# Performance work log

Measured on AMD Instinct MI355X. Metric: run time of the kernel, lower is better.

## Reference

```python
import jax, jax.numpy as jnp
import numpy as np

N = 50000      # nodes
E = 800000     # edges
F_IN = 256     # feat_dim
H = 256        # hidden dim (both layers)
L = 128        # latent dim
BN_EPS = 1e-5


def setup_inputs() -> dict:
    key = jax.random.key(0)
    ks = jax.random.split(key, 16)
    x = jax.random.normal(ks[0], (N, F_IN), dtype=jnp.float32)
    edge_index = jax.random.randint(ks[1], (2, E), 0, N, dtype=jnp.int32)
    s = 0.05
    return {
        "x": x,
        "edge_index": edge_index,
        "W0": s * jax.random.normal(ks[2], (F_IN, H), jnp.float32),
        "b0": jnp.zeros((H,), jnp.float32),
        "gamma0": jnp.ones((H,), jnp.float32),
        "beta0": jnp.zeros((H,), jnp.float32),
        "W1": s * jax.random.normal(ks[3], (H, H), jnp.float32),
        "b1": jnp.zeros((H,), jnp.float32),
        "gamma1": jnp.ones((H,), jnp.float32),
        "beta1": jnp.zeros((H,), jnp.float32),
        "W_mu": s * jax.random.normal(ks[4], (H, L), jnp.float32),
        "b_mu": jnp.zeros((L,), jnp.float32),
        "W_lv": s * jax.random.normal(ks[5], (H, L), jnp.float32),
        "b_lv": jnp.zeros((L,), jnp.float32),
    }


def _gcn_conv(h, src, dst, coef, W, b):
    # h' = W h, then symmetric-normalized scatter-add aggregation (PyG GCNConv)
    h = h @ W                                   # [N, H]
    msg = h[src] * coef                         # gather + scale, [E+N, H]
    out = jax.ops.segment_sum(msg, dst, num_segments=N)
    return out + b


def _bn(h, gamma, beta):
    # BatchNorm1d over node dimension (training-mode batch statistics)
    m = h.mean(axis=0)
    v = h.var(axis=0)
    return (h - m) * jax.lax.rsqrt(v + BN_EPS) * gamma + beta


def reference(x, edge_index, W0, b0, gamma0, beta0, W1, b1, gamma1, beta1,
              W_mu, b_mu, W_lv, b_lv):
    loops = jnp.arange(N, dtype=edge_index.dtype)
    src = jnp.concatenate([edge_index[0], loops])   # with self-loops
    dst = jnp.concatenate([edge_index[1], loops])
    deg = jax.ops.segment_sum(jnp.ones((E + N,), x.dtype), dst, num_segments=N)
    dinv = jnp.where(deg > 0, jax.lax.rsqrt(jnp.maximum(deg, 1.0)), 0.0)
    coef = (dinv[src] * dinv[dst])[:, None]          # [E+N, 1]

    h = jax.nn.relu(_bn(_gcn_conv(x, src, dst, coef, W0, b0), gamma0, beta0))
    h = jax.nn.relu(_bn(_gcn_conv(h, src, dst, coef, W1, b1), gamma1, beta1))
    # dropout is identity at inference
    mu = h @ W_mu + b_mu
    logvar = h @ W_lv + b_lv
    return mu, logvar
```

## Files before the change

kernel.cpp:

```cpp
#include <hip/hip_runtime.h>
#include <hip/hip_bf16.h>

#define NN 50000
#define NP 50001
#define NE 800000
#define FD 256
#define LD 128
#define BN_EPS 1e-5f
#define NEPAD (NE + 7 * NN + 16)
#define CNT_BLKS 3125
#define ORD_BLKS 196
#define SCAN_BLKS 49

typedef __bf16 bf16_t;
typedef bf16_t bf16x8 __attribute__((ext_vector_type(8)));
typedef float f32x4 __attribute__((ext_vector_type(4)));
typedef float f32x2 __attribute__((ext_vector_type(2)));
typedef int i32x2 __attribute__((ext_vector_type(2)));
typedef int i32x4 __attribute__((ext_vector_type(4)));
typedef unsigned int u32x4 __attribute__((ext_vector_type(4)));
typedef unsigned short u16x8 __attribute__((ext_vector_type(8)));

__global__ __launch_bounds__(256) void k_countw(
    const int* __restrict__ dst, int* __restrict__ cnt,
    const float* __restrict__ W0, const float* __restrict__ W1,
    const float* __restrict__ Wmu, const float* __restrict__ bmu,
    const float* __restrict__ Wlv, const float* __restrict__ blv,
    bf16_t* __restrict__ W0s, bf16_t* __restrict__ W1s,
    bf16_t* __restrict__ Whs, float* __restrict__ biash,
    bf16_t* __restrict__ g16, bf16_t* __restrict__ agg16) {
  int b = blockIdx.x, t = threadIdx.x;
  if (b < CNT_BLKS) {
    int i = b * 256 + t;
    if (i < NE) atomicAdd(&cnt[dst[i]], 1);
  } else {
    int k = b - CNT_BLKS, n = t;
    int chunk = (n >> 4) * 8 + (k >> 5);
    int slot = ((k >> 3) & 3) * 16 + (n & 15);
    int idx = chunk * 512 + slot * 8 + (k & 7);
    W0s[idx] = (bf16_t)W0[k * 256 + n];
    W1s[idx] = (bf16_t)W1[k * 256 + n];
    float wh = (n < 128) ? Wmu[k * 128 + n] : Wlv[k * 128 + (n - 128)];
    Whs[idx] = (bf16_t)wh;
    if (k == 0) biash[n] = (n < 128) ? bmu[n] : blv[n - 128];
    if (k == 1) {
      int ss = n >> 6, j = n & 63;
      g16[((size_t)ss * NP + NN) * 64 + j] = (bf16_t)0.f;
      agg16[((size_t)ss * NP + NN) * 64 + j] = (bf16_t)0.f;
    }
  }
}

__global__ __launch_bounds__(256) void k_scanA(const int* __restrict__ cnt,
                                               int* __restrict__ row_ptr,
                                               int* __restrict__ partials,
                                               float* __restrict__ dinv) {
  __shared__ int ws[4];
  int b = blockIdx.x, t = threadIdx.x;
  int base = b * 1024 + t * 4;
  int vals[4];
#pragma unroll
  for (int j = 0; j < 4; ++j) {
    int deg = (base + j < NN) ? cnt[base + j] : 0;
    vals[j] = (base + j < NN) ? ((deg + 7) & ~7) : 0;
    if (base + j < NN) dinv[base + j] = rsqrtf(1.0f + (float)deg);
  }
  int tsum = vals[0] + vals[1] + vals[2] + vals[3];
  int lane = t & 63, wid = t >> 6;
  int x = tsum;
#pragma unroll
  for (int off = 1; off < 64; off <<= 1) {
    int y = __shfl_up(x, off, 64);
    if (lane >= off) x += y;
  }
  if (lane == 63) ws[wid] = x;
  __syncthreads();
  int woff = 0;
  for (int w = 0; w < wid; ++w) woff += ws[w];
  int run = woff + x - tsum;
#pragma unroll
  for (int j = 0; j < 4; ++j) {
    if (base + j < NN) row_ptr[base + j] = run;
    run += vals[j];
  }
  if (t == 255) partials[b] = woff + x;
}

__global__ void k_scanB(int* __restrict__ partials, int* __restrict__ row_ptr) {
  int lane = threadIdx.x;
  int v = (lane < SCAN_BLKS) ? partials[lane] : 0;
  int x = v;
#pragma unroll
  for (int off = 1; off < 64; off <<= 1) {
    int y = __shfl_up(x, off, 64);
    if (lane >= off) x += y;
  }
  if (lane < SCAN_BLKS) partials[lane] = x - v;
  if (lane == SCAN_BLKS - 1) row_ptr[NN] = x;
}

__global__ __launch_bounds__(256) void k_scanC(int* __restrict__ row_ptr,
                                               const int* __restrict__ partials,
                                               const int* __restrict__ cnt,
                                               unsigned short* __restrict__ col,
                                               int* __restrict__ hist) {
  __shared__ int lh[64];
  int b = blockIdx.x, t = threadIdx.x;
  if (t < 64) lh[t] = 0;
  __syncthreads();
  int off = partials[b];
  int base = b * 1024 + t * 4;
#pragma unroll
  for (int j = 0; j < 4; ++j)
    if (base + j < NN) {
      int deg = cnt[base + j];
      int rp = row_ptr[base + j] + off;
      row_ptr[base + j] = rp;
      int pd = (deg + 7) & ~7;
      for (int p = deg; p < pd; ++p) col[rp + p] = (unsigned short)NN;
      int it = pd >> 3;
      if (it > 63) it = 63;
      atomicAdd(&lh[63 - it], 1);
    }
  __syncthreads();
  if (t < 64 && lh[t]) atomicAdd(&hist[t], lh[t]);
}

__global__ __launch_bounds__(256) void k_fillorder(
    const int* __restrict__ src, const int* __restrict__ dst,
    const int* __restrict__ row_ptr, int* __restrict__ cursor,
    unsigned short* __restrict__ col, const int* __restrict__ cnt,
    const float* __restrict__ dinv, const int* __restrict__ hist,
    int* __restrict__ rank, int* __restrict__ order, i32x2* __restrict__ desc,
    float* __restrict__ dinvp) {
  int b = blockIdx.x, t = threadIdx.x;
  if (b < CNT_BLKS) {
    int i = b * 256 + t;
    if (i < NE) {
      int d = dst[i];
      int p = atomicAdd(&cursor[d], 1);
      col[row_ptr[d] + p] = (unsigned short)src[i];
    }
  } else {
    __shared__ int lcnt[64];
    __shared__ int gbase[64];
    __shared__ int sc[64];
    if (t < 64) {
      lcnt[t] = 0;
      int v = hist[t];
      int x = v;
#pragma unroll
      for (int off = 1; off < 64; off <<= 1) {
        int y = __shfl_up(x, off, 64);
        if (t >= off) x += y;
      }
      sc[t] = x - v;
    }
    __syncthreads();
    int i = (b - CNT_BLKS) * 256 + t;
    int bin = 0, rloc = 0, pd = 0;
    bool valid = (i < NN);
    if (valid) {
      pd = (cnt[i] + 7) & ~7;
      int it = pd >> 3;
      if (it > 63) it = 63;
      bin = 63 - it;
      rloc = atomicAdd(&lcnt[bin], 1);
    }
    __syncthreads();
    if (t < 64 && lcnt[t]) gbase[t] = sc[t] + atomicAdd(&rank[t], lcnt[t]);
    __syncthreads();
    if (valid) {
      int p = gbase[bin] + rloc;
      order[p] = i;
      int rp = row_ptr[i];
      desc[p] = (i32x2){rp, rp + pd};
      dinvp[p] = dinv[i];
    }
  }
}

__global__ __launch_bounds__(512) void k_mgemm(
    const void* __restrict__ Ap, int a_f32, const bf16_t* __restrict__ Wswz,
    bf16_t* __restrict__ Cb, float* __restrict__ Cf, int M,
    const float* __restrict__ stats, const float* __restrict__ gamma,
    const float* __restrict__ beta, const float* __restrict__ row_scale,
    const float* __restrict__ col_bias, int split) {
  __shared__ bf16_t Ws[64 * 512];
  __shared__ float bnsc_l[256], bnsh_l[256];
  const int tid = threadIdx.x;
  const int half = blockIdx.y;
  {
    const bf16_t* srcW = Wswz + (size_t)half * 64 * 512;
    bf16x8 wraw[8];
#pragma unroll
    for (int i = 0; i < 8; ++i)
      wraw[i] = *(const bf16x8*)&srcW[(i * 512 + tid) * 8];
#pragma unroll
    for (int i = 0; i < 8; ++i) *(bf16x8*)&Ws[(i * 512 + tid) * 8] = wraw[i];
  }
  if (stats && tid < 256) {
    float mean = stats[tid] * (1.0f / NN);
    float var = stats[256 + tid] * (1.0f / NN) - mean * mean;
    float rs = rsqrtf(var + BN_EPS);
    float sc = gamma[tid] * rs;
    bnsc_l[tid] = sc;
    bnsh_l[tid] = beta[tid] - mean * sc;
  }
  __syncthreads();

  const int wave = tid >> 6, lane = tid & 63;
  const int m = lane & 15, q = lane >> 4;
  const int row0 = blockIdx.x * 128 + wave * 16;
  const int rg = row0 + m;
  const int rc = rg < M ? rg : M - 1;

  bf16x8 af[8];
  if (a_f32) {
    const float* p = (const float*)Ap + (size_t)rc * 256 + q * 8;
    float4 f0[8], f1[8];
#pragma unroll
    for (int kb = 0; kb < 8; ++kb) {
      f0[kb] = *(const float4*)(p + kb * 32);
      f1[kb] = *(const float4*)(p + kb * 32 + 4);
    }
#pragma unroll
    for (int kb = 0; kb < 8; ++kb) {
      bf16x8 fr;
      fr[0] = (bf16_t)f0[kb].x; fr[1] = (bf16_t)f0[kb].y;
      fr[2] = (bf16_t)f0[kb].z; fr[3] = (bf16_t)f0[kb].w;
      fr[4] = (bf16_t)f1[kb].x; fr[5] = (bf16_t)f1[kb].y;
      fr[6] = (bf16_t)f1[kb].z; fr[7] = (bf16_t)f1[kb].w;
      af[kb] = fr;
    }
  } else {
    const bf16_t* pA = (const bf16_t*)Ap;
    bf16x8 raw[8];
#pragma unroll
    for (int kb = 0; kb < 8; ++kb)
      raw[kb] = *(const bf16x8*)&pA[((size_t)(kb >> 1) * NP + rc) * 64 +
                                    (kb & 1) * 32 + q * 8];
#pragma unroll
    for (int kb = 0; kb < 8; ++kb) {
      float s[8], h[8];
      if (stats) {
        float4 s0 = *(const float4*)&bnsc_l[kb * 32 + q * 8];
        float4 s1 = *(const float4*)&bnsc_l[kb * 32 + q * 8 + 4];
        float4 h0 = *(const float4*)&bnsh_l[kb * 32 + q * 8];
        float4 h1 = *(const float4*)&bnsh_l[kb * 32 + q * 8 + 4];
        s[0] = s0.x; s[1] = s0.y; s[2] = s0.z; s[3] = s0.w;
        s[4] = s1.x; s[5] = s1.y; s[6] = s1.z; s[7] = s1.w;
        h[0] = h0.x; h[1] = h0.y; h[2] = h0.z; h[3] = h0.w;
        h[4] = h1.x; h[5] = h1.y; h[6] = h1.z; h[7] = h1.w;
      }
      bf16x8 r = raw[kb];
      bf16x8 fr;
#pragma unroll
      for (int j = 0; j < 8; ++j) {
        float v = (float)r[j];
        if (stats) v = fmaxf(fmaf(v, s[j], h[j]), 0.f);
        fr[j] = (bf16_t)v;
      }
      af[kb] = fr;
    }
  }

  f32x4 acc[8] = {};
#pragma unroll
  for (int nt = 0; nt < 8; ++nt) {
#pragma unroll
    for (int kb = 0; kb < 8; ++kb) {
      bf16x8 b = *(const bf16x8*)&Ws[(nt * 8 + kb) * 512 + lane * 8];
      acc[nt] =
          __builtin_amdgcn_mfma_f32_16x16x32_bf16(af[kb], b, acc[nt], 0, 0, 0);
    }
  }

#pragma unroll
  for (int r = 0; r < 4; ++r) {
    int row = row0 + q * 4 + r;
    if (row >= M) continue;
    float rs = row_scale ? row_scale[row] : 1.0f;
#pragma unroll
    for (int nt = 0; nt < 8; ++nt) {
      int col = half * 128 + nt * 16 + m;
      float v = acc[nt][r] * rs;
      if (col_bias) v += col_bias[col];
      if (Cb) {
        Cb[((size_t)(col >> 6) * NP + row) * 64 + (col & 63)] = (bf16_t)v;
      } else if (!split) {
        Cf[(size_t)row * 256 + col] = v;
      } else {
        if (col < 128)
          Cf[(size_t)row * 128 + col] = v;
        else
          Cf[(size_t)(M + row) * 128 + (col - 128)] = v;
      }
    }
  }
}

#define ACCUM8(A, d)                                             \
  A[0] += (f32x2){__uint_as_float(d[0] << 16),                   \
                  __uint_as_float(d[0] & 0xffff0000u)};          \
  A[1] += (f32x2){__uint_as_float(d[1] << 16),                   \
                  __uint_as_float(d[1] & 0xffff0000u)};          \
  A[2] += (f32x2){__uint_as_float(d[2] << 16),                   \
                  __uint_as_float(d[2] & 0xffff0000u)};          \
  A[3] += (f32x2){__uint_as_float(d[3] << 16),                   \
                  __uint_as_float(d[3] & 0xffff0000u)};

__global__ __launch_bounds__(256) void k_spmm(
    const bf16_t* __restrict__ g, const int* __restrict__ order,
    const i32x2* __restrict__ desc, const unsigned short* __restrict__ col,
    const float* __restrict__ dinvp, bf16_t* __restrict__ out,
    float* __restrict__ stats) {
  __shared__ float sbuf[32][64];
  const int s = blockIdx.x & 3;
  const int grp = blockIdx.x >> 2;
  const int team = threadIdx.x >> 3, tl = threadIdx.x & 7;
  const int slotA = grp * 64 + team * 2;
  const u32x4* gu = (const u32x4*)(g + (size_t)s * NP * 64);
  float s1[8] = {}, s2[8] = {};
  if (slotA < NN) {
    f32x2 accA[4] = {}, accB[4] = {};
    i32x2 o2 = *(const i32x2*)&order[slotA];
    i32x4 d4 = *(const i32x4*)&desc[slotA];
    f32x2 dv2 = *(const f32x2*)&dinvp[slotA];
    int dstA = o2[0], dstB = o2[1];
    int bA = d4[0], eA = d4[1], bB = d4[2], eB = d4[3];
    {
      u32x4 dA = gu[(size_t)dstA * 8 + tl];
      u32x4 dB = gu[(size_t)dstB * 8 + tl];
      ACCUM8(accA, dA)
      ACCUM8(accB, dB)
    }
    u16x8 cA = {}, cB = {};
    if (bA < eA) cA = __builtin_nontemporal_load((const u16x8*)&col[bA]);
    if (bB < eB) cB = __builtin_nontemporal_load((const u16x8*)&col[bB]);
    while (bA < eA && bB < eB) {
      u32x4 wa0 = gu[(size_t)cA[0] * 8 + tl];
      u32x4 wa1 = gu[(size_t)cA[1] * 8 + tl];
      u32x4 wa2 = gu[(size_t)cA[2] * 8 + tl];
      u32x4 wa3 = gu[(size_t)cA[3] * 8 + tl];
      u32x4 wa4 = gu[(size_t)cA[4] * 8 + tl];
      u32x4 wa5 = gu[(size_t)cA[5] * 8 + tl];
      u32x4 wa6 = gu[(size_t)cA[6] * 8 + tl];
      u32x4 wa7 = gu[(size_t)cA[7] * 8 + tl];
      u32x4 wb0 = gu[(size_t)cB[0] * 8 + tl];
      u32x4 wb1 = gu[(size_t)cB[1] * 8 + tl];
      u32x4 wb2 = gu[(size_t)cB[2] * 8 + tl];
      u32x4 wb3 = gu[(size_t)cB[3] * 8 + tl];
      u32x4 wb4 = gu[(size_t)cB[4] * 8 + tl];
      u32x4 wb5 = gu[(size_t)cB[5] * 8 + tl];
      u32x4 wb6 = gu[(size_t)cB[6] * 8 + tl];
      u32x4 wb7 = gu[(size_t)cB[7] * 8 + tl];
      int bnA = bA + 8, bnB = bB + 8;
      u16x8 cnA = {}, cnB = {};
      if (bnA < eA) cnA = __builtin_nontemporal_load((const u16x8*)&col[bnA]);
      if (bnB < eB) cnB = __builtin_nontemporal_load((const u16x8*)&col[bnB]);
      ACCUM8(accA, wa0) ACCUM8(accA, wa1) ACCUM8(accA, wa2) ACCUM8(accA, wa3)
      ACCUM8(accA, wa4) ACCUM8(accA, wa5) ACCUM8(accA, wa6) ACCUM8(accA, wa7)
      ACCUM8(accB, wb0) ACCUM8(accB, wb1) ACCUM8(accB, wb2) ACCUM8(accB, wb3)
      ACCUM8(accB, wb4) ACCUM8(accB, wb5) ACCUM8(accB, wb6) ACCUM8(accB, wb7)
      cA = cnA;
      cB = cnB;
      bA = bnA;
      bB = bnB;
    }
    while (bA < eA) {
      u32x4 w0 = gu[(size_t)cA[0] * 8 + tl];
      u32x4 w1 = gu[(size_t)cA[1] * 8 + tl];
      u32x4 w2 = gu[(size_t)cA[2] * 8 + tl];
      u32x4 w3 = gu[(size_t)cA[3] * 8 + tl];
      u32x4 w4 = gu[(size_t)cA[4] * 8 + tl];
      u32x4 w5 = gu[(size_t)cA[5] * 8 + tl];
      u32x4 w6 = gu[(size_t)cA[6] * 8 + tl];
      u32x4 w7 = gu[(size_t)cA[7] * 8 + tl];
      int bn = bA + 8;
      u16x8 cn = {};
      if (bn < eA) cn = __builtin_nontemporal_load((const u16x8*)&col[bn]);
      ACCUM8(accA, w0) ACCUM8(accA, w1) ACCUM8(accA, w2) ACCUM8(accA, w3)
      ACCUM8(accA, w4) ACCUM8(accA, w5) ACCUM8(accA, w6) ACCUM8(accA, w7)
      cA = cn;
      bA = bn;
    }
    while (bB < eB) {
      u32x4 w0 = gu[(size_t)cB[0] * 8 + tl];
      u32x4 w1 = gu[(size_t)cB[1] * 8 + tl];
      u32x4 w2 = gu[(size_t)cB[2] * 8 + tl];
      u32x4 w3 = gu[(size_t)cB[3] * 8 + tl];
      u32x4 w4 = gu[(size_t)cB[4] * 8 + tl];
      u32x4 w5 = gu[(size_t)cB[5] * 8 + tl];
      u32x4 w6 = gu[(size_t)cB[6] * 8 + tl];
      u32x4 w7 = gu[(size_t)cB[7] * 8 + tl];
      int bn = bB + 8;
      u16x8 cn = {};
      if (bn < eB) cn = __builtin_nontemporal_load((const u16x8*)&col[bn]);
      ACCUM8(accB, w0) ACCUM8(accB, w1) ACCUM8(accB, w2) ACCUM8(accB, w3)
      ACCUM8(accB, w4) ACCUM8(accB, w5) ACCUM8(accB, w6) ACCUM8(accB, w7)
      cB = cn;
      bB = bn;
    }
    float dvA = dv2[0], dvB = dv2[1];
    bf16x8 ovA, ovB;
#pragma unroll
    for (int j = 0; j < 8; ++j) {
      ovA[j] = (bf16_t)(accA[j >> 1][j & 1] * dvA);
      ovB[j] = (bf16_t)(accB[j >> 1][j & 1] * dvB);
    }
    __builtin_nontemporal_store(
        ovA, (bf16x8*)&out[((size_t)s * NP + dstA) * 64 + (size_t)tl * 8]);
    __builtin_nontemporal_store(
        ovB, (bf16x8*)&out[((size_t)s * NP + dstB) * 64 + (size_t)tl * 8]);
#pragma unroll
    for (int j = 0; j < 8; ++j) {
      float va = (float)ovA[j], vb = (float)ovB[j];
      s1[j] += va + vb;
      s2[j] = fmaf(va, va, s2[j]);
      s2[j] = fmaf(vb, vb, s2[j]);
    }
  }
#pragma unroll
  for (int j = 0; j < 8; ++j) sbuf[team][tl * 8 + j] = s1[j];
  __syncthreads();
  if (threadIdx.x < 64) {
    float tot = 0.f;
#pragma unroll
    for (int w = 0; w < 32; ++w) tot += sbuf[w][threadIdx.x];
    atomicAdd(&stats[s * 64 + threadIdx.x], tot);
  }
  __syncthreads();
#pragma unroll
  for (int j = 0; j < 8; ++j) sbuf[team][tl * 8 + j] = s2[j];
  __syncthreads();
  if (threadIdx.x < 64) {
    float tot = 0.f;
#pragma unroll
    for (int w = 0; w < 32; ++w) tot += sbuf[w][threadIdx.x];
    atomicAdd(&stats[256 + s * 64 + threadIdx.x], tot);
  }
}

extern "C" void kernel_launch(void* const* d_in, const int* in_sizes, int n_in,
                              void* d_out, int out_size, void* d_ws, size_t ws_size,
                              hipStream_t stream) {
  const float* x = (const float*)d_in[0];
  const int* ei = (const int*)d_in[1];
  const int* esrc = ei;
  const int* edst = ei + NE;
  const float* W0 = (const float*)d_in[2];
  const float* gamma0 = (const float*)d_in[4];
  const float* beta0 = (const float*)d_in[5];
  const float* W1 = (const float*)d_in[6];
  const float* gamma1 = (const float*)d_in[8];
  const float* beta1 = (const float*)d_in[9];
  const float* W_mu = (const float*)d_in[10];
  const float* b_mu = (const float*)d_in[11];
  const float* W_lv = (const float*)d_in[12];
  const float* b_lv = (const float*)d_in[13];
  float* out = (float*)d_out;

  bf16_t* g16 = (bf16_t*)d_ws;
  bf16_t* agg16 = g16 + (size_t)4 * NP * 64;
  int* cnt = (int*)(agg16 + (size_t)4 * NP * 64);
  int* cursor = cnt + NN;
  float* statsAll = (float*)(cursor + NN);
  int* hist = (int*)(statsAll + 1024);
  int* rank = hist + 64;
  float* dinv = (float*)(rank + 64);
  float* biash = dinv + NN;
  bf16_t* W0s = (bf16_t*)(biash + 256);
  bf16_t* W1s = W0s + 256 * 256;
  bf16_t* Whs = W1s + 256 * 256;
  int* row_ptr = (int*)(Whs + 256 * 256);
  int* order = row_ptr + NN + 4;
  float* dinvp = (float*)(order + NN);
  i32x2* desc = (i32x2*)(dinvp + NN);
  unsigned short* col = (unsigned short*)(desc + NN);
  int* partials = (int*)(col + NEPAD);

  hipMemsetAsync(cnt, 0, (2 * NN + 1024 + 128) * sizeof(int), stream);
  k_countw<<<CNT_BLKS + 256, 256, 0, stream>>>(edst, cnt, W0, W1, W_mu, b_mu,
                                               W_lv, b_lv, W0s, W1s, Whs,
                                               biash, g16, agg16);
  k_scanA<<<SCAN_BLKS, 256, 0, stream>>>(cnt, row_ptr, partials, dinv);
  k_scanB<<<1, 64, 0, stream>>>(partials, row_ptr);
  k_scanC<<<SCAN_BLKS, 256, 0, stream>>>(row_ptr, partials, cnt, col, hist);
  k_fillorder<<<CNT_BLKS + ORD_BLKS, 256, 0, stream>>>(
      esrc, edst, row_ptr, cursor, col, cnt, dinv, hist, rank, order, desc,
      dinvp);

  dim3 gg((NN + 127) / 128, 2);
  const int SPMM_BLKS = 4 * ((NN + 63) / 64);

  k_mgemm<<<gg, 512, 0, stream>>>(x, 1, W0s, g16, nullptr, NN, nullptr, nullptr,
                                  nullptr, dinv, nullptr, 0);
  k_spmm<<<SPMM_BLKS, 256, 0, stream>>>(g16, order, desc, col, dinvp, agg16,
                                        statsAll);

  k_mgemm<<<gg, 512, 0, stream>>>(agg16, 0, W1s, g16, nullptr, NN, statsAll,
                                  gamma0, beta0, dinv, nullptr, 0);
  k_spmm<<<SPMM_BLKS, 256, 0, stream>>>(g16, order, desc, col, dinvp, agg16,
                                        statsAll + 512);

  k_mgemm<<<gg, 512, 0, stream>>>(agg16, 0, Whs, nullptr, out, NN,
                                  statsAll + 512, gamma1, beta1, nullptr, biash,
                                  1);
}
```

Measured before the change: 374.0 us.

## Fuse CSR fill and ordering with first-layer GEMM in one interleaved launch

Merges the edge-fill/node-ordering kernel and the first X@W0 GEMM into one launch. Fill, order and GEMM blocks are interleaved so the atomic-bound scatter and the MFMA-bound GEMM can share the GPU at the same time. The cursor is now seeded with absolute row offsets in the scan, which removes the row_ptr lookup per edge. The fill blocks must reserve the GEMM's large shared-memory array, which may lower their occupancy. The general GEMM loses its fp32-input and no-stats branches.

```diff
diff --git a/kernel.cpp b/kernel.cpp
--- a/kernel.cpp
+++ b/kernel.cpp
@@ -9,8 +9,11 @@
 #define BN_EPS 1e-5f
 #define NEPAD (NE + 7 * NN + 16)
 #define CNT_BLKS 3125
-#define ORD_BLKS 196
 #define SCAN_BLKS 49
+#define FILL_BLKS 1563
+#define ORD2_BLKS 98
+#define MG_BLKS 782
+#define FG_BLKS (FILL_BLKS + ORD2_BLKS + MG_BLKS)
 
 typedef __bf16 bf16_t;
 typedef bf16_t bf16x8 __attribute__((ext_vector_type(8)));
@@ -102,6 +105,7 @@
 __global__ __launch_bounds__(256) void k_scanC(int* __restrict__ row_ptr,
                                                const int* __restrict__ partials,
                                                const int* __restrict__ cnt,
+                                               int* __restrict__ cursor,
                                                unsigned short* __restrict__ col,
                                                int* __restrict__ hist) {
   __shared__ int lh[64];
@@ -116,6 +120,7 @@
       int deg = cnt[base + j];
       int rp = row_ptr[base + j] + off;
       row_ptr[base + j] = rp;
+      cursor[base + j] = rp;
       int pd = (deg + 7) & ~7;
       for (int p = deg; p < pd; ++p) col[rp + p] = (unsigned short)NN;
       int it = pd >> 3;
@@ -126,62 +131,133 @@
   if (t < 64 && lh[t]) atomicAdd(&hist[t], lh[t]);
 }
 
-__global__ __launch_bounds__(256) void k_fillorder(
+__global__ __launch_bounds__(512) void k_fillgemm(
     const int* __restrict__ src, const int* __restrict__ dst,
-    const int* __restrict__ row_ptr, int* __restrict__ cursor,
-    unsigned short* __restrict__ col, const int* __restrict__ cnt,
+    int* __restrict__ cursor, unsigned short* __restrict__ col,
+    const int* __restrict__ cnt, const int* __restrict__ row_ptr,
     const float* __restrict__ dinv, const int* __restrict__ hist,
     int* __restrict__ rank, int* __restrict__ order, i32x2* __restrict__ desc,
-    float* __restrict__ dinvp) {
-  int b = blockIdx.x, t = threadIdx.x;
-  if (b < CNT_BLKS) {
-    int i = b * 256 + t;
-    if (i < NE) {
-      int d = dst[i];
-      int p = atomicAdd(&cursor[d], 1);
-      col[row_ptr[d] + p] = (unsigned short)src[i];
-    }
-  } else {
-    __shared__ int lcnt[64];
-    __shared__ int gbase[64];
-    __shared__ int sc[64];
-    if (t < 64) {
-      lcnt[t] = 0;
-      int v = hist[t];
-      int x = v;
-#pragma unroll
-      for (int off = 1; off < 64; off <<= 1) {
-        int y = __shfl_up(x, off, 64);
-        if (t >= off) x += y;
-      }
-      sc[t] = x - v;
-    }
+    float* __restrict__ dinvp, const float* __restrict__ x,
+    const bf16_t* __restrict__ W0s, bf16_t* __restrict__ g16) {
+  __shared__ bf16_t Ws[64 * 512];
+  const int nb = blockIdx.x, t = threadIdx.x;
+  const bool isMg = (nb % 3 == 2) && (nb / 3) < MG_BLKS;
+  if (!isMg) {
+    int mgBefore = (nb + 1) / 3;
+    if (mgBefore > MG_BLKS) mgBefore = MG_BLKS;
+    int fo = nb - mgBefore;
+    if (fo < FILL_BLKS) {
+      int i = fo * 512 + t;
+      if (i < NE) {
+        int d = dst[i];
+        int p = atomicAdd(&cursor[d], 1);
+        col[p] = (unsigned short)src[i];
+      }
+    } else {
+      __shared__ int lcnt[64];
+      __shared__ int gbase[64];
+      __shared__ int sc[64];
+      if (t < 64) {
+        lcnt[t] = 0;
+        int v = hist[t];
+        int xx = v;
+#pragma unroll
+        for (int off = 1; off < 64; off <<= 1) {
+          int y = __shfl_up(xx, off, 64);
+          if (t >= off) xx += y;
+        }
+        sc[t] = xx - v;
+      }
+      __syncthreads();
+      int i = (fo - FILL_BLKS) * 512 + t;
+      int bin = 0, rloc = 0, pd = 0;
+      bool valid = (i < NN);
+      if (valid) {
+        pd = (cnt[i] + 7) & ~7;
+        int it = pd >> 3;
+        if (it > 63) it = 63;
+        bin = 63 - it;
+        rloc = atomicAdd(&lcnt[bin], 1);
+      }
+      __syncthreads();
+      if (t < 64 && lcnt[t]) gbase[t] = sc[t] + atomicAdd(&rank[t], lcnt[t]);
+      __syncthreads();
+      if (valid) {
+        int p = gbase[bin] + rloc;
+        order[p] = i;
+        int rp = row_ptr[i];
+        desc[p] = (i32x2){rp, rp + pd};
+        dinvp[p] = dinv[i];
+      }
+    }
+    return;
+  }
+  {
+    int mb = nb / 3;
+    int bx = mb >> 1, half = mb & 1;
+    const bf16_t* srcW = W0s + (size_t)half * 64 * 512;
+    bf16x8 wraw[8];
+#pragma unroll
+    for (int i = 0; i < 8; ++i)
+      wraw[i] = *(const bf16x8*)&srcW[(i * 512 + t) * 8];
+#pragma unroll
+    for (int i = 0; i < 8; ++i) *(bf16x8*)&Ws[(i * 512 + t) * 8] = wraw[i];
     __syncthreads();
-    int i = (b - CNT_BLKS) * 256 + t;
-    int bin = 0, rloc = 0, pd = 0;
-    bool valid = (i < NN);
-    if (valid) {
-      pd = (cnt[i] + 7) & ~7;
-      int it = pd >> 3;
-      if (it > 63) it = 63;
-      bin = 63 - it;
-      rloc = atomicAdd(&lcnt[bin], 1);
-    }
-    __syncthreads();
-    if (t < 64 && lcnt[t]) gbase[t] = sc[t] + atomicAdd(&rank[t], lcnt[t]);
-    __syncthreads();
-    if (valid) {
-      int p = gbase[bin] + rloc;
-      order[p] = i;
-      int rp = row_ptr[i];
-      desc[p] = (i32x2){rp, rp + pd};
-      dinvp[p] = dinv[i];
+
+    const int wave = t >> 6, lane = t & 63;
+    const int m = lane & 15, q = lane >> 4;
+    const int row0 = bx * 128 + wave * 16;
+    const int rg = row0 + m;
+    const int rc = rg < NN ? rg : NN - 1;
+
+    const float* p = x + (size_t)rc * 256 + q * 8;
+    bf16x8 af[8];
+    {
+      float4 f0[8], f1[8];
+#pragma unroll
+      for (int kb = 0; kb < 8; ++kb) {
+        f0[kb] = *(const float4*)(p + kb * 32);
+        f1[kb] = *(const float4*)(p + kb * 32 + 4);
+      }
+#pragma unroll
+      for (int kb = 0; kb < 8; ++kb) {
+        bf16x8 fr;
+        fr[0] = (bf16_t)f0[kb].x; fr[1] = (bf16_t)f0[kb].y;
+        fr[2] = (bf16_t)f0[kb].z; fr[3] = (bf16_t)f0[kb].w;
+        fr[4] = (bf16_t)f1[kb].x; fr[5] = (bf16_t)f1[kb].y;
+        fr[6] = (bf16_t)f1[kb].z; fr[7] = (bf16_t)f1[kb].w;
+        af[kb] = fr;
+      }
+    }
+
+    f32x4 acc[8] = {};
+#pragma unroll
+    for (int nt = 0; nt < 8; ++nt) {
+#pragma unroll
+      for (int kb = 0; kb < 8; ++kb) {
+        bf16x8 bfr = *(const bf16x8*)&Ws[(nt * 8 + kb) * 512 + lane * 8];
+        acc[nt] = __builtin_amdgcn_mfma_f32_16x16x32_bf16(af[kb], bfr, acc[nt],
+                                                          0, 0, 0);
+      }
+    }
+
+#pragma unroll
+    for (int r = 0; r < 4; ++r) {
+      int row = row0 + q * 4 + r;
+      if (row >= NN) continue;
+      float rs = dinv[row];
+#pragma unroll
+      for (int nt = 0; nt < 8; ++nt) {
+        int c = half * 128 + nt * 16 + m;
+        g16[((size_t)(c >> 6) * NP + row) * 64 + (c & 63)] =
+            (bf16_t)(acc[nt][r] * rs);
+      }
     }
   }
 }
 
 __global__ __launch_bounds__(512) void k_mgemm(
-    const void* __restrict__ Ap, int a_f32, const bf16_t* __restrict__ Wswz,
+    const void* __restrict__ Ap, const bf16_t* __restrict__ Wswz,
     bf16_t* __restrict__ Cb, float* __restrict__ Cf, int M,
     const float* __restrict__ stats, const float* __restrict__ gamma,
     const float* __restrict__ beta, const float* __restrict__ row_scale,
@@ -199,7 +275,7 @@
 #pragma unroll
     for (int i = 0; i < 8; ++i) *(bf16x8*)&Ws[(i * 512 + tid) * 8] = wraw[i];
   }
-  if (stats && tid < 256) {
+  if (tid < 256) {
     float mean = stats[tid] * (1.0f / NN);
     float var = stats[256 + tid] * (1.0f / NN) - mean * mean;
     float rs = rsqrtf(var + BN_EPS);
@@ -215,26 +291,9 @@
   const int rg = row0 + m;
   const int rc = rg < M ? rg : M - 1;
 
+  const bf16_t* pA = (const bf16_t*)Ap;
   bf16x8 af[8];
-  if (a_f32) {
-    const float* p = (const float*)Ap + (size_t)rc * 256 + q * 8;
-    float4 f0[8], f1[8];
-#pragma unroll
-    for (int kb = 0; kb < 8; ++kb) {
-      f0[kb] = *(const float4*)(p + kb * 32);
-      f1[kb] = *(const float4*)(p + kb * 32 + 4);
-    }
-#pragma unroll
-    for (int kb = 0; kb < 8; ++kb) {
-      bf16x8 fr;
-      fr[0] = (bf16_t)f0[kb].x; fr[1] = (bf16_t)f0[kb].y;
-      fr[2] = (bf16_t)f0[kb].z; fr[3] = (bf16_t)f0[kb].w;
-      fr[4] = (bf16_t)f1[kb].x; fr[5] = (bf16_t)f1[kb].y;
-      fr[6] = (bf16_t)f1[kb].z; fr[7] = (bf16_t)f1[kb].w;
-      af[kb] = fr;
-    }
-  } else {
-    const bf16_t* pA = (const bf16_t*)Ap;
+  {
     bf16x8 raw[8];
 #pragma unroll
     for (int kb = 0; kb < 8; ++kb)
@@ -243,22 +302,20 @@
 #pragma unroll
     for (int kb = 0; kb < 8; ++kb) {
       float s[8], h[8];
-      if (stats) {
-        float4 s0 = *(const float4*)&bnsc_l[kb * 32 + q * 8];
-        float4 s1 = *(const float4*)&bnsc_l[kb * 32 + q * 8 + 4];
-        float4 h0 = *(const float4*)&bnsh_l[kb * 32 + q * 8];
-        float4 h1 = *(const float4*)&bnsh_l[kb * 32 + q * 8 + 4];
-        s[0] = s0.x; s[1] = s0.y; s[2] = s0.z; s[3] = s0.w;
-        s[4] = s1.x; s[5] = s1.y; s[6] = s1.z; s[7] = s1.w;
-        h[0] = h0.x; h[1] = h0.y; h[2] = h0.z; h[3] = h0.w;
-        h[4] = h1.x; h[5] = h1.y; h[6] = h1.z; h[7] = h1.w;
-      }
+      float4 s0 = *(const float4*)&bnsc_l[kb * 32 + q * 8];
+      float4 s1 = *(const float4*)&bnsc_l[kb * 32 + q * 8 + 4];
+      float4 h0 = *(const float4*)&bnsh_l[kb * 32 + q * 8];
+      float4 h1 = *(const float4*)&bnsh_l[kb * 32 + q * 8 + 4];
+      s[0] = s0.x; s[1] = s0.y; s[2] = s0.z; s[3] = s0.w;
+      s[4] = s1.x; s[5] = s1.y; s[6] = s1.z; s[7] = s1.w;
+      h[0] = h0.x; h[1] = h0.y; h[2] = h0.z; h[3] = h0.w;
+      h[4] = h1.x; h[5] = h1.y; h[6] = h1.z; h[7] = h1.w;
       bf16x8 r = raw[kb];
       bf16x8 fr;
 #pragma unroll
       for (int j = 0; j < 8; ++j) {
         float v = (float)r[j];
-        if (stats) v = fmaxf(fmaf(v, s[j], h[j]), 0.f);
+        v = fmaxf(fmaf(v, s[j], h[j]), 0.f);
         fr[j] = (bf16_t)v;
       }
       af[kb] = fr;
@@ -486,25 +543,23 @@
                                                biash, g16, agg16);
   k_scanA<<<SCAN_BLKS, 256, 0, stream>>>(cnt, row_ptr, partials, dinv);
   k_scanB<<<1, 64, 0, stream>>>(partials, row_ptr);
-  k_scanC<<<SCAN_BLKS, 256, 0, stream>>>(row_ptr, partials, cnt, col, hist);
-  k_fillorder<<<CNT_BLKS + ORD_BLKS, 256, 0, stream>>>(
-      esrc, edst, row_ptr, cursor, col, cnt, dinv, hist, rank, order, desc,
-      dinvp);
+  k_scanC<<<SCAN_BLKS, 256, 0, stream>>>(row_ptr, partials, cnt, cursor, col,
+                                         hist);
+  k_fillgemm<<<FG_BLKS, 512, 0, stream>>>(esrc, edst, cursor, col, cnt,
+                                          row_ptr, dinv, hist, rank, order,
+                                          desc, dinvp, x, W0s, g16);
 
   dim3 gg((NN + 127) / 128, 2);
   const int SPMM_BLKS = 4 * ((NN + 63) / 64);
 
-  k_mgemm<<<gg, 512, 0, stream>>>(x, 1, W0s, g16, nullptr, NN, nullptr, nullptr,
-                                  nullptr, dinv, nullptr, 0);
   k_spmm<<<SPMM_BLKS, 256, 0, stream>>>(g16, order, desc, col, dinvp, agg16,
                                         statsAll);
 
-  k_mgemm<<<gg, 512, 0, stream>>>(agg16, 0, W1s, g16, nullptr, NN, statsAll,
+  k_mgemm<<<gg, 512, 0, stream>>>(agg16, W1s, g16, nullptr, NN, statsAll,
                                   gamma0, beta0, dinv, nullptr, 0);
   k_spmm<<<SPMM_BLKS, 256, 0, stream>>>(g16, order, desc, col, dinvp, agg16,
                                         statsAll + 512);
 
-  k_mgemm<<<gg, 512, 0, stream>>>(agg16, 0, Whs, nullptr, out, NN,
-                                  statsAll + 512, gamma1, beta1, nullptr, biash,
-                                  1);
-}
+  k_mgemm<<<gg, 512, 0, stream>>>(agg16, Whs, nullptr, out, NN, statsAll + 512,
+                                  gamma1, beta1, nullptr, biash, 1);
+}
```

Measured after the change: 350.7 us. 6.2% less time.
